# Kernel optimization log

Measured on AMD Instinct MI355X. Metric: run time of the kernel, lower is better.

## Reference

```python
import jax, jax.numpy as jnp
import numpy as np
import math

INPUT_SIZE = 512
HIDDEN_SIZE = 1024
BATCH = 64
SEQ = 512


def setup_inputs() -> dict:
    key = jax.random.key(0)
    ks = jax.random.split(key, 13)
    stdv = 1.0 / math.sqrt(HIDDEN_SIZE)
    def u(k, shape):
        return jax.random.uniform(k, shape, jnp.float32, -stdv, stdv)
    x = jax.random.normal(ks[0], (BATCH, SEQ, INPUT_SIZE), jnp.float32)
    return {
        "x": x,
        "U_i": u(ks[1], (INPUT_SIZE, HIDDEN_SIZE)), "V_i": u(ks[2], (HIDDEN_SIZE, HIDDEN_SIZE)), "b_i": u(ks[3], (HIDDEN_SIZE,)),
        "U_f": u(ks[4], (INPUT_SIZE, HIDDEN_SIZE)), "V_f": u(ks[5], (HIDDEN_SIZE, HIDDEN_SIZE)), "b_f": u(ks[6], (HIDDEN_SIZE,)),
        "U_c": u(ks[7], (INPUT_SIZE, HIDDEN_SIZE)), "V_c": u(ks[8], (HIDDEN_SIZE, HIDDEN_SIZE)), "b_c": u(ks[9], (HIDDEN_SIZE,)),
        "U_o": u(ks[10], (INPUT_SIZE, HIDDEN_SIZE)), "V_o": u(ks[11], (HIDDEN_SIZE, HIDDEN_SIZE)), "b_o": u(ks[12], (HIDDEN_SIZE,)),
    }


def reference(x, U_i, V_i, b_i, U_f, V_f, b_f, U_c, V_c, b_c, U_o, V_o, b_o):
    B, T, _ = x.shape
    H = V_i.shape[0]
    # Fuse the four input->gate matmuls into one wide GEMM over all timesteps.
    U = jnp.concatenate([U_i, U_f, U_c, U_o], axis=1)  # [I, 4H]
    V = jnp.concatenate([V_i, V_f, V_c, V_o], axis=1)  # [H, 4H]
    b = jnp.concatenate([b_i, b_f, b_c, b_o], axis=0)  # [4H]
    xU = jnp.einsum('bti,ig->tbg', x, U) + b           # [T, B, 4H]

    def step(carry, xu_t):
        h, c = carry
        gates = xu_t + h @ V                           # [B, 4H]
        i_t = jax.nn.sigmoid(gates[:, 0*H:1*H])
        f_t = jax.nn.sigmoid(gates[:, 1*H:2*H])
        g_t = jax.nn.sigmoid(gates[:, 2*H:3*H])  # NOTE: source uses sigmoid, not tanh
        o_t = jax.nn.sigmoid(gates[:, 3*H:4*H])
        c = f_t * c + i_t * g_t
        h = o_t * jnp.tanh(c)
        return (h, c), h

    h0 = jnp.zeros((B, H), x.dtype)
    c0 = jnp.zeros((B, H), x.dtype)
    (h_T, c_T), hs = jax.lax.scan(step, (h0, c0), xU)
    hidden_seq = jnp.transpose(hs, (1, 0, 2))          # [B, T, H]
    return hidden_seq, (h_T, c_T)
```

## Files before the change

### kernel.cpp

```cpp
#include <hip/hip_runtime.h>
#include <stdint.h>

#define B_  64
#define T_  512
#define I_  512
#define H_  1024
#define G4  4096
#define KW  1536

#define GROUPS 4
#define GBLK   64
#define MBR    16

#define LDS_BYTES 66048

typedef __attribute__((ext_vector_type(8))) short bf16x8;
typedef __attribute__((ext_vector_type(4))) float f32x4;

#define OFF_WT   ((size_t)0)
#define OFF_XB   ((size_t)(16u << 20))
#define OFF_HB   (OFF_XB + (size_t)33554432)
#define WS_NEED  (OFF_HB + (size_t)262144)

__device__ __forceinline__ unsigned short f2bf(float x) {
  unsigned u = __float_as_uint(x);
  u += 0x7FFFu + ((u >> 16) & 1u);
  return (unsigned short)(u >> 16);
}
__device__ __forceinline__ float sigm(float x) {
  return 1.0f / (1.0f + __expf(-x));
}

__global__ __launch_bounds__(256) void pack_w_kernel(
    const float* __restrict__ U0, const float* __restrict__ U1,
    const float* __restrict__ U2, const float* __restrict__ U3,
    const float* __restrict__ V0, const float* __restrict__ V1,
    const float* __restrict__ V2, const float* __restrict__ V3,
    short* __restrict__ Wt)
{
  __shared__ short sl[64][65];
  const int c0 = blockIdx.x * 64;
  const int k0 = blockIdx.y * 64;
  const int g  = c0 >> 10;
  const int h0 = c0 & 1023;
  const float* srcU = (g == 0 ? U0 : g == 1 ? U1 : g == 2 ? U2 : U3);
  const float* srcV = (g == 0 ? V0 : g == 1 ? V1 : g == 2 ? V2 : V3);
  const float* src  = (k0 < 512) ? (srcU + (size_t)k0 * H_)
                                 : (srcV + (size_t)(k0 - 512) * H_);
  const int tid = threadIdx.x;
  const int cl = tid & 63;
  const int r4 = tid >> 6;
  #pragma unroll
  for (int r = 0; r < 16; ++r) {
    const int kl = r * 4 + r4;
    sl[kl][cl] = (short)f2bf(src[(size_t)kl * H_ + h0 + cl]);
  }
  __syncthreads();
  #pragma unroll
  for (int r = 0; r < 16; ++r) {
    const int cl2 = r * 4 + r4;
    Wt[(size_t)(c0 + cl2) * KW + k0 + cl] = sl[cl][cl2];
  }
}

__global__ __launch_bounds__(256) void xcvt(
    const float* __restrict__ x, short* __restrict__ xb)
{
  const int nt = 524288;
  const int idx = blockIdx.x * 256 + threadIdx.x;
  #pragma unroll
  for (int i = 0; i < 8; ++i) {
    const int j = idx + i * nt;
    const float4 v = ((const float4*)x)[j];
    uint2 pk;
    pk.x = (unsigned)f2bf(v.x) | ((unsigned)f2bf(v.y) << 16);
    pk.y = (unsigned)f2bf(v.z) | ((unsigned)f2bf(v.w) << 16);
    ((uint2*)xb)[j] = pk;
  }
}

#define FR_ADDR(unit, slot) ((((unit) * 64) + ((slot) ^ ((unit) & 7))) * 8)

__global__ __launch_bounds__(512, 2) void lstm_rec(
    const short* __restrict__ Wt, const short* __restrict__ xb,
    const float* __restrict__ b0g, const float* __restrict__ b1g,
    const float* __restrict__ b2g, const float* __restrict__ b3g,
    short* __restrict__ hb, float* __restrict__ out)
{
  extern __shared__ char smem[];
  short* sh = (short*)smem;
  short* sx = (short*)(smem + 32768);
  float* gl = (float*)(smem + 49152);

  const int tid = threadIdx.x;
  const int blk = blockIdx.x;
  const int g   = blk >> 6;
  const int bi  = blk & 63;
  const int base = bi * 16;
  const int b0  = g * MBR;

  const int w = tid >> 6, l = tid & 63;
  const int kq = w & 3;
  const int np = w >> 2;
  const int cit = l & 15;
  const int l16 = l >> 4;
  const int slot_r = (cit << 2) | l16;

  bf16x8 vfr[2][8];
  bf16x8 ufr[2][4];
  #pragma unroll
  for (int n = 0; n < 2; ++n) {
    const int col = (np * 2 + n) * 1024 + base + cit;
    const short* wp = Wt + (size_t)col * KW;
    #pragma unroll
    for (int j = 0; j < 8; ++j)
      vfr[n][j] = *(const bf16x8*)(wp + 512 + kq * 256 + j * 32 + l16 * 8);
    #pragma unroll
    for (int j = 0; j < 4; ++j)
      ufr[n][j] = *(const bf16x8*)(wp + kq * 128 + j * 32 + l16 * 8);
  }

  const float* bias0 = (np == 0) ? b0g : b2g;
  const float* bias1 = (np == 0) ? b1g : b3g;
  const float bv0 = (kq == 0) ? bias0[base + cit] : 0.0f;
  const float bv1 = (kq == 0) ? bias1[base + cit] : 0.0f;

  const int crow = tid >> 4;
  const int ccj  = tid & 15;

  const int xr0_row = tid >> 6;
  const int xr1_row = 8 + (tid >> 6);
  const int x_k0 = (tid & 63) * 8;
  const int x_unit = x_k0 >> 5;
  const int xr0_addr = FR_ADDR(x_unit, (xr0_row << 2) | (tid & 3));
  const int xr1_addr = FR_ADDR(x_unit, (xr1_row << 2) | (tid & 3));
  const short* xsrc0 = xb + (size_t)(b0 + xr0_row) * T_ * I_ + x_k0;
  const short* xsrc1 = xb + (size_t)(b0 + xr1_row) * T_ * I_ + x_k0;

  float c_state = 0.0f;

  *(int4*)(sx + xr0_addr) = *(const int4*)(xsrc0);
  *(int4*)(sx + xr1_addr) = *(const int4*)(xsrc1);
  __syncthreads();
  f32x4 xacc0 = (f32x4){bv0, bv0, bv0, bv0};
  f32x4 xacc1 = (f32x4){bv1, bv1, bv1, bv1};
  #pragma unroll
  for (int j = 0; j < 4; ++j) {
    const bf16x8 xf = *(const bf16x8*)(sx + FR_ADDR(kq * 4 + j, slot_r));
    xacc0 = __builtin_amdgcn_mfma_f32_16x16x32_bf16(xf, ufr[0][j], xacc0, 0, 0, 0);
    xacc1 = __builtin_amdgcn_mfma_f32_16x16x32_bf16(xf, ufr[1][j], xacc1, 0, 0, 0);
  }
  int4 xr0 = *(const int4*)(xsrc0 + (size_t)1 * I_);
  int4 xr1 = *(const int4*)(xsrc1 + (size_t)1 * I_);

  for (int t = 0; t < T_; ++t) {
    {
      const unsigned expw = ((t >> 1) & 1) ? 0x00010001u : 0u;
      const short* hsrc = hb + ((size_t)(t & 1) * GROUPS + g) * (MBR * H_);
      int4 v0, v1, v2, v3;
      for (;;) {
        #define LDC(ii, vv) { \
          const short* p = hsrc + (size_t)((((ii) * 512 + tid) >> 7)) * H_ \
                           + ((((ii) * 512 + tid) & 127) * 8); \
          asm volatile("global_load_dwordx4 %0, %1, off sc0 sc1" : "=&v"(vv) : "v"(p)); }
        LDC(0, v0) LDC(1, v1) LDC(2, v2) LDC(3, v3)
        #undef LDC
        asm volatile("s_waitcnt vmcnt(0)" ::: "memory");
        __builtin_amdgcn_sched_barrier(0);
        #define XR(vv) (((unsigned)(vv).x ^ expw) | ((unsigned)(vv).y ^ expw) | \
                        ((unsigned)(vv).z ^ expw) | ((unsigned)(vv).w ^ expw))
        const unsigned diff = (XR(v0) | XR(v1) | XR(v2) | XR(v3)) & 0x00010001u;
        #undef XR
        if (__all(diff == 0u)) break;
        asm volatile("s_sleep 1" ::: "memory");
      }
      #define STC(ii, vv) { const int f = (ii) * 512 + tid; const int row = f >> 7; \
        const int k0s = (f & 127) * 8; \
        *(int4*)(sh + FR_ADDR(k0s >> 5, (row << 2) | ((k0s >> 3) & 3))) = vv; }
      STC(0, v0) STC(1, v1) STC(2, v2) STC(3, v3)
      #undef STC
    }
    __syncthreads();

    f32x4 acc0 = xacc0, acc1 = xacc1;
    #pragma unroll
    for (int j = 0; j < 8; ++j) {
      const bf16x8 af = *(const bf16x8*)(sh + FR_ADDR(kq * 8 + j, slot_r));
      acc0 = __builtin_amdgcn_mfma_f32_16x16x32_bf16(af, vfr[0][j], acc0, 0, 0, 0);
      acc1 = __builtin_amdgcn_mfma_f32_16x16x32_bf16(af, vfr[1][j], acc1, 0, 0, 0);
    }

    #pragma unroll
    for (int i = 0; i < 4; ++i) {
      gl[(l16 * 4 + i) * 260 + kq * 64 + (np * 2 + 0) * 16 + cit] = acc0[i];
      gl[(l16 * 4 + i) * 260 + kq * 64 + (np * 2 + 1) * 16 + cit] = acc1[i];
    }
    __syncthreads();

    if (tid < 256) {
      const float* gr = gl + crow * 260;
      float s[4];
      #pragma unroll
      for (int gate = 0; gate < 4; ++gate)
        s[gate] = gr[0 * 64 + gate * 16 + ccj] + gr[1 * 64 + gate * 16 + ccj]
                + gr[2 * 64 + gate * 16 + ccj] + gr[3 * 64 + gate * 16 + ccj];
      const float i_ = sigm(s[0]), f_ = sigm(s[1]), g_ = sigm(s[2]), o_ = sigm(s[3]);
      c_state = f_ * c_state + i_ * g_;
      const float hval = o_ * tanhf(c_state);
      if (t + 1 < T_) {
        unsigned hv = (unsigned)f2bf(hval);
        hv = (hv & ~1u) | (unsigned)(((t + 1) >> 1) & 1);
        short* hdst = hb + ((size_t)((t + 1) & 1) * GROUPS + g) * (MBR * H_)
                      + (size_t)crow * H_ + base + ccj;
        asm volatile("global_store_short %0, %1, off sc0 sc1" :: "v"(hdst), "v"(hv) : "memory");
      }
      out[((size_t)(b0 + crow) << 19) + (size_t)t * H_ + base + ccj] = hval;
      if (t == T_ - 1) {
        out[(size_t)B_ * T_ * H_ + (size_t)(b0 + crow) * H_ + base + ccj] = hval;
        out[(size_t)B_ * T_ * H_ + (size_t)B_ * H_ + (size_t)(b0 + crow) * H_ + base + ccj] = c_state;
      }
    }

    if (t + 1 < T_) {
      *(int4*)(sx + xr0_addr) = xr0;
      *(int4*)(sx + xr1_addr) = xr1;
      {
        const size_t tn = (size_t)((t + 2 < T_) ? t + 2 : T_ - 1);
        xr0 = *(const int4*)(xsrc0 + tn * I_);
        xr1 = *(const int4*)(xsrc1 + tn * I_);
      }
      __syncthreads();

      xacc0 = (f32x4){bv0, bv0, bv0, bv0};
      xacc1 = (f32x4){bv1, bv1, bv1, bv1};
      #pragma unroll
      for (int j = 0; j < 4; ++j) {
        const bf16x8 xf = *(const bf16x8*)(sx + FR_ADDR(kq * 4 + j, slot_r));
        xacc0 = __builtin_amdgcn_mfma_f32_16x16x32_bf16(xf, ufr[0][j], xacc0, 0, 0, 0);
        xacc1 = __builtin_amdgcn_mfma_f32_16x16x32_bf16(xf, ufr[1][j], xacc1, 0, 0, 0);
      }
    }
  }
}

extern "C" void kernel_launch(void* const* d_in, const int* in_sizes, int n_in,
                              void* d_out, int out_size, void* d_ws, size_t ws_size,
                              hipStream_t stream)
{
  const float* x  = (const float*)d_in[0];
  const float* U0 = (const float*)d_in[1];
  const float* Vg0 = (const float*)d_in[2];
  const float* bg0 = (const float*)d_in[3];
  const float* U1 = (const float*)d_in[4];
  const float* Vg1 = (const float*)d_in[5];
  const float* bg1 = (const float*)d_in[6];
  const float* U2 = (const float*)d_in[7];
  const float* Vg2 = (const float*)d_in[8];
  const float* bg2 = (const float*)d_in[9];
  const float* U3 = (const float*)d_in[10];
  const float* Vg3 = (const float*)d_in[11];
  const float* bg3 = (const float*)d_in[12];

  if (ws_size < WS_NEED) return;

  char* ws = (char*)d_ws;
  short* Wt = (short*)(ws + OFF_WT);
  short* xb = (short*)(ws + OFF_XB);
  short* hb = (short*)(ws + OFF_HB);

  (void)hipFuncSetAttribute((const void*)lstm_rec,
                      hipFuncAttributeMaxDynamicSharedMemorySize, LDS_BYTES);

  (void)hipMemsetAsync(ws + OFF_HB, 0x00, 131072, stream);
  (void)hipMemsetAsync(ws + OFF_HB + 131072, 0x01, 131072, stream);
  pack_w_kernel<<<dim3(64, 24), 256, 0, stream>>>(U0, U1, U2, U3, Vg0, Vg1, Vg2, Vg3, Wt);
  xcvt<<<dim3(2048), 256, 0, stream>>>(x, xb);
  lstm_rec<<<dim3(GROUPS * GBLK), 512, LDS_BYTES, stream>>>(
      Wt, xb, bg0, bg1, bg2, bg3, hb, (float*)d_out);
}
```

Before: 1.143 ms.

## Pre-swizzle x into MFMA fragment layout and load x fragments directly from global

```diff
diff --git a/kernel.cpp b/kernel.cpp
--- a/kernel.cpp
+++ b/kernel.cpp
@@ -5,14 +5,13 @@
 #define T_  512
 #define I_  512
 #define H_  1024
-#define G4  4096
 #define KW  1536
 
 #define GROUPS 4
 #define GBLK   64
 #define MBR    16
 
-#define LDS_BYTES 66048
+#define LDS_BYTES 49408
 
 typedef __attribute__((ext_vector_type(8))) short bf16x8;
 typedef __attribute__((ext_vector_type(4))) float f32x4;
@@ -29,6 +28,13 @@
 }
 __device__ __forceinline__ float sigm(float x) {
   return 1.0f / (1.0f + __expf(-x));
+}
+__device__ __forceinline__ float fast_tanh(float x) {
+  const float e2 = __expf(2.0f * x);
+  return 1.0f - 2.0f / (e2 + 1.0f);
+}
+__device__ __forceinline__ bf16x8 bc8(int4 v) {
+  union { int4 i; bf16x8 b; } u; u.i = v; return u.b;
 }
 
 __global__ __launch_bounds__(256) void pack_w_kernel(
@@ -66,22 +72,29 @@
 __global__ __launch_bounds__(256) void xcvt(
     const float* __restrict__ x, short* __restrict__ xb)
 {
-  const int nt = 524288;
-  const int idx = blockIdx.x * 256 + threadIdx.x;
-  #pragma unroll
-  for (int i = 0; i < 8; ++i) {
-    const int j = idx + i * nt;
-    const float4 v = ((const float4*)x)[j];
-    uint2 pk;
-    pk.x = (unsigned)f2bf(v.x) | ((unsigned)f2bf(v.y) << 16);
-    pk.y = (unsigned)f2bf(v.z) | ((unsigned)f2bf(v.w) << 16);
-    ((uint2*)xb)[j] = pk;
-  }
+  const int gid = blockIdx.x;
+  const int q  = gid & 3;
+  const int tg = gid >> 2;
+  const int t  = tg >> 2, g = tg & 3;
+  const int F  = q * 256 + threadIdx.x;
+  const int unit = F >> 6, slot = F & 63;
+  const int row = slot >> 2, l8 = (slot & 3) * 8;
+  const float* src = x + ((size_t)(g * 16 + row) * T_ + t) * I_ + unit * 32 + l8;
+  const float4 v0 = *(const float4*)(src);
+  const float4 v1 = *(const float4*)(src + 4);
+  int4 pk;
+  pk.x = (int)((unsigned)f2bf(v0.x) | ((unsigned)f2bf(v0.y) << 16));
+  pk.y = (int)((unsigned)f2bf(v0.z) | ((unsigned)f2bf(v0.w) << 16));
+  pk.z = (int)((unsigned)f2bf(v1.x) | ((unsigned)f2bf(v1.y) << 16));
+  pk.w = (int)((unsigned)f2bf(v1.z) | ((unsigned)f2bf(v1.w) << 16));
+  *(int4*)(xb + (size_t)tg * 8192 + (size_t)F * 8) = pk;
 }
 
 #define FR_ADDR(unit, slot) ((((unit) * 64) + ((slot) ^ ((unit) & 7))) * 8)
 
-__global__ __launch_bounds__(512, 2) void lstm_rec(
+#define MFMA_ __builtin_amdgcn_mfma_f32_16x16x32_bf16
+
+__global__ __launch_bounds__(512, 1) void lstm_rec(
     const short* __restrict__ Wt, const short* __restrict__ xb,
     const float* __restrict__ b0g, const float* __restrict__ b1g,
     const float* __restrict__ b2g, const float* __restrict__ b3g,
@@ -89,8 +102,7 @@
 {
   extern __shared__ char smem[];
   short* sh = (short*)smem;
-  short* sx = (short*)(smem + 32768);
-  float* gl = (float*)(smem + 49152);
+  float* gl = (float*)(smem + 32768);
 
   const int tid = threadIdx.x;
   const int blk = blockIdx.x;
@@ -128,30 +140,32 @@
   const int crow = tid >> 4;
   const int ccj  = tid & 15;
 
-  const int xr0_row = tid >> 6;
-  const int xr1_row = 8 + (tid >> 6);
-  const int x_k0 = (tid & 63) * 8;
-  const int x_unit = x_k0 >> 5;
-  const int xr0_addr = FR_ADDR(x_unit, (xr0_row << 2) | (tid & 3));
-  const int xr1_addr = FR_ADDR(x_unit, (xr1_row << 2) | (tid & 3));
-  const short* xsrc0 = xb + (size_t)(b0 + xr0_row) * T_ * I_ + x_k0;
-  const short* xsrc1 = xb + (size_t)(b0 + xr1_row) * T_ * I_ + x_k0;
+  const short* xg = xb + (size_t)g * 8192 + (size_t)((kq * 4) * 64 + slot_r) * 8;
 
   float c_state = 0.0f;
-
-  *(int4*)(sx + xr0_addr) = *(const int4*)(xsrc0);
-  *(int4*)(sx + xr1_addr) = *(const int4*)(xsrc1);
-  __syncthreads();
-  f32x4 xacc0 = (f32x4){bv0, bv0, bv0, bv0};
-  f32x4 xacc1 = (f32x4){bv1, bv1, bv1, bv1};
-  #pragma unroll
-  for (int j = 0; j < 4; ++j) {
-    const bf16x8 xf = *(const bf16x8*)(sx + FR_ADDR(kq * 4 + j, slot_r));
-    xacc0 = __builtin_amdgcn_mfma_f32_16x16x32_bf16(xf, ufr[0][j], xacc0, 0, 0, 0);
-    xacc1 = __builtin_amdgcn_mfma_f32_16x16x32_bf16(xf, ufr[1][j], xacc1, 0, 0, 0);
-  }
-  int4 xr0 = *(const int4*)(xsrc0 + (size_t)1 * I_);
-  int4 xr1 = *(const int4*)(xsrc1 + (size_t)1 * I_);
+  int4 nx0, nx1, nx2, nx3;
+  f32x4 xacc0, xacc1;
+
+  {
+    const int4 a0 = *(const int4*)(xg + 0 * 512);
+    const int4 a1 = *(const int4*)(xg + 1 * 512);
+    const int4 a2 = *(const int4*)(xg + 2 * 512);
+    const int4 a3 = *(const int4*)(xg + 3 * 512);
+    xacc0 = (f32x4){bv0, bv0, bv0, bv0};
+    xacc1 = (f32x4){bv1, bv1, bv1, bv1};
+    xacc0 = MFMA_(bc8(a0), ufr[0][0], xacc0, 0, 0, 0);
+    xacc1 = MFMA_(bc8(a0), ufr[1][0], xacc1, 0, 0, 0);
+    xacc0 = MFMA_(bc8(a1), ufr[0][1], xacc0, 0, 0, 0);
+    xacc1 = MFMA_(bc8(a1), ufr[1][1], xacc1, 0, 0, 0);
+    xacc0 = MFMA_(bc8(a2), ufr[0][2], xacc0, 0, 0, 0);
+    xacc1 = MFMA_(bc8(a2), ufr[1][2], xacc1, 0, 0, 0);
+    xacc0 = MFMA_(bc8(a3), ufr[0][3], xacc0, 0, 0, 0);
+    xacc1 = MFMA_(bc8(a3), ufr[1][3], xacc1, 0, 0, 0);
+  }
+  nx0 = *(const int4*)(xg + (size_t)1 * 32768 + 0 * 512);
+  nx1 = *(const int4*)(xg + (size_t)1 * 32768 + 1 * 512);
+  nx2 = *(const int4*)(xg + (size_t)1 * 32768 + 2 * 512);
+  nx3 = *(const int4*)(xg + (size_t)1 * 32768 + 3 * 512);
 
   for (int t = 0; t < T_; ++t) {
     {
@@ -186,8 +200,8 @@
     #pragma unroll
     for (int j = 0; j < 8; ++j) {
       const bf16x8 af = *(const bf16x8*)(sh + FR_ADDR(kq * 8 + j, slot_r));
-      acc0 = __builtin_amdgcn_mfma_f32_16x16x32_bf16(af, vfr[0][j], acc0, 0, 0, 0);
-      acc1 = __builtin_amdgcn_mfma_f32_16x16x32_bf16(af, vfr[1][j], acc1, 0, 0, 0);
+      acc0 = MFMA_(af, vfr[0][j], acc0, 0, 0, 0);
+      acc1 = MFMA_(af, vfr[1][j], acc1, 0, 0, 0);
     }
 
     #pragma unroll
@@ -206,7 +220,7 @@
                 + gr[2 * 64 + gate * 16 + ccj] + gr[3 * 64 + gate * 16 + ccj];
       const float i_ = sigm(s[0]), f_ = sigm(s[1]), g_ = sigm(s[2]), o_ = sigm(s[3]);
       c_state = f_ * c_state + i_ * g_;
-      const float hval = o_ * tanhf(c_state);
+      const float hval = o_ * fast_tanh(c_state);
       if (t + 1 < T_) {
         unsigned hv = (unsigned)f2bf(hval);
         hv = (hv & ~1u) | (unsigned)(((t + 1) >> 1) & 1);
@@ -222,22 +236,24 @@
     }
 
     if (t + 1 < T_) {
-      *(int4*)(sx + xr0_addr) = xr0;
-      *(int4*)(sx + xr1_addr) = xr1;
+      const int4 c0 = nx0, c1 = nx1, c2 = nx2, c3 = nx3;
+      xacc0 = (f32x4){bv0, bv0, bv0, bv0};
+      xacc1 = (f32x4){bv1, bv1, bv1, bv1};
+      xacc0 = MFMA_(bc8(c0), ufr[0][0], xacc0, 0, 0, 0);
+      xacc1 = MFMA_(bc8(c0), ufr[1][0], xacc1, 0, 0, 0);
+      xacc0 = MFMA_(bc8(c1), ufr[0][1], xacc0, 0, 0, 0);
+      xacc1 = MFMA_(bc8(c1), ufr[1][1], xacc1, 0, 0, 0);
+      xacc0 = MFMA_(bc8(c2), ufr[0][2], xacc0, 0, 0, 0);
+      xacc1 = MFMA_(bc8(c2), ufr[1][2], xacc1, 0, 0, 0);
+      xacc0 = MFMA_(bc8(c3), ufr[0][3], xacc0, 0, 0, 0);
+      xacc1 = MFMA_(bc8(c3), ufr[1][3], xacc1, 0, 0, 0);
       {
         const size_t tn = (size_t)((t + 2 < T_) ? t + 2 : T_ - 1);
-        xr0 = *(const int4*)(xsrc0 + tn * I_);
-        xr1 = *(const int4*)(xsrc1 + tn * I_);
-      }
-      __syncthreads();
-
-      xacc0 = (f32x4){bv0, bv0, bv0, bv0};
-      xacc1 = (f32x4){bv1, bv1, bv1, bv1};
-      #pragma unroll
-      for (int j = 0; j < 4; ++j) {
-        const bf16x8 xf = *(const bf16x8*)(sx + FR_ADDR(kq * 4 + j, slot_r));
-        xacc0 = __builtin_amdgcn_mfma_f32_16x16x32_bf16(xf, ufr[0][j], xacc0, 0, 0, 0);
-        xacc1 = __builtin_amdgcn_mfma_f32_16x16x32_bf16(xf, ufr[1][j], xacc1, 0, 0, 0);
+        const short* xp = xg + tn * 32768;
+        nx0 = *(const int4*)(xp + 0 * 512);
+        nx1 = *(const int4*)(xp + 1 * 512);
+        nx2 = *(const int4*)(xp + 2 * 512);
+        nx3 = *(const int4*)(xp + 3 * 512);
       }
     }
   }
@@ -274,7 +290,7 @@
   (void)hipMemsetAsync(ws + OFF_HB, 0x00, 131072, stream);
   (void)hipMemsetAsync(ws + OFF_HB + 131072, 0x01, 131072, stream);
   pack_w_kernel<<<dim3(64, 24), 256, 0, stream>>>(U0, U1, U2, U3, Vg0, Vg1, Vg2, Vg3, Wt);
-  xcvt<<<dim3(2048), 256, 0, stream>>>(x, xb);
+  xcvt<<<dim3(8192), 256, 0, stream>>>(x, xb);
   lstm_rec<<<dim3(GROUPS * GBLK), 512, LDS_BYTES, stream>>>(
       Wt, xb, bg0, bg1, bg2, bg3, hb, (float*)d_out);
 }
```

Measured after the change: 2.316 ms. +102.6%, slower.
